# Kernel optimization log

Measured on AMD Instinct MI355X. Metric: run time of the kernel, lower is better.

The kernel has to match this reference:

```python
import jax, jax.numpy as jnp
import numpy as np

B, S, D, H = 2, 2048, 1024, 16
HD = D // H  # head_size = 64

def setup_inputs() -> dict:
    key = jax.random.key(0)
    ks = jax.random.split(key, 8)
    sc = 0.02
    return {
        "q": jax.random.normal(ks[0], (B, S, D), jnp.float32),
        "k": jax.random.normal(ks[1], (B, S, D), jnp.float32),
        "v": jax.random.normal(ks[2], (B, S, D), jnp.float32),
        "padding_mask": jnp.zeros((B, 1, 1, S), jnp.float32),
        "Wq": jax.random.normal(ks[3], (D, D), jnp.float32) * sc,
        "bq": jnp.zeros((D,), jnp.float32),
        "Wk": jax.random.normal(ks[4], (D, D), jnp.float32) * sc,
        "bk": jnp.zeros((D,), jnp.float32),
        "Wv": jax.random.normal(ks[5], (D, D), jnp.float32) * sc,
        "bv": jnp.zeros((D,), jnp.float32),
        "Wo": jax.random.normal(ks[6], (D, D), jnp.float32) * sc,
        "bo": jnp.zeros((D,), jnp.float32),
    }

def reference(q, k, v, padding_mask, Wq, bq, Wk, bk, Wv, bv, Wo, bo):
    b = q.shape[0]
    qh = (q @ Wq + bq).reshape(b, -1, H, HD)
    kh = (k @ Wk + bk).reshape(b, -1, H, HD)
    vh = (v @ Wv + bv).reshape(b, -1, H, HD)
    # [B, H, Sq, Sk] scores, materialized as in the original
    qk = jnp.einsum('bjhd,bkhd->bhjk', qh, kh) / jnp.sqrt(jnp.float32(HD))
    qk = qk + padding_mask * -1e12
    attn = jax.nn.softmax(qk, axis=-1)
    qkv = jnp.einsum('bhjk,bkhd->bjhd', attn, vh).reshape(b, -1, D)
    return qkv @ Wo + bo
```

## Files before the change

### kernel.cpp

```cpp
#include <hip/hip_runtime.h>
#include <math.h>

typedef __bf16 bf16_t;
typedef __bf16 bf16x8 __attribute__((ext_vector_type(8)));
typedef __bf16 bf16x4v __attribute__((ext_vector_type(4)));
typedef float f32x4 __attribute__((ext_vector_type(4)));
typedef float f32x16 __attribute__((ext_vector_type(16)));

#define LOG2E 1.4426950408889634f
#define MBIAS_C (-1e12f * LOG2E)

#if __has_builtin(__builtin_amdgcn_exp2f)
#define EXP2F(x) __builtin_amdgcn_exp2f(x)
#else
#define EXP2F(x) exp2f(x)
#endif

typedef __attribute__((address_space(1))) const unsigned int g_u32;
typedef __attribute__((address_space(3))) unsigned int l_u32;
__device__ __forceinline__ void load_lds_16B(const void* g, void* l){
  __builtin_amdgcn_global_load_lds((g_u32*)g, (l_u32*)l, 16, 0, 0);
}

__device__ __forceinline__ f32x16 zero16(){
  f32x16 z;
  #pragma unroll
  for (int i = 0; i < 16; i++) z[i] = 0.f;
  return z;
}

typedef union { bf16x4v b4; uint2 u2; } pk8;
typedef union { uint2 h[2]; bf16x8 b8; } pk16;
typedef union { float4 f4[4]; f32x16 v; } cinit_t;

__global__ __launch_bounds__(256) void prep_kernel(const float* __restrict__ q,
                                                   const float* __restrict__ k,
                                                   const float* __restrict__ v,
                                                   const float* __restrict__ Wq,
                                                   const float* __restrict__ Wk,
                                                   const float* __restrict__ Wv,
                                                   const float* __restrict__ Wo,
                                                   bf16_t* __restrict__ qkvin,
                                                   bf16_t* __restrict__ Wcat,
                                                   bf16_t* __restrict__ Wot,
                                                   int cast_blocks){
  __shared__ float T[32][33];
  int id = blockIdx.x, tid = threadIdx.x;
  if (id < cast_blocks){
    int z = id >> 12;
    int i = (id & 4095) * 256 + tid;
    const float* x = (z == 0) ? q : (z == 1) ? k : v;
    float4 f = reinterpret_cast<const float4*>(x)[i];
    bf16x4v w;
    w[0] = (bf16_t)f.x; w[1] = (bf16_t)f.y; w[2] = (bf16_t)f.z; w[3] = (bf16_t)f.w;
    reinterpret_cast<bf16x4v*>(qkvin + (size_t)z * 4194304)[i] = w;
  } else {
    int wid = id - cast_blocks;
    int z = wid >> 10, t = wid & 1023;
    int k0 = (t >> 5) * 32, n0 = (t & 31) * 32;
    int x = tid & 31, y = tid >> 5;
    const float* W = (z == 0) ? Wq : (z == 1) ? Wk : (z == 2) ? Wv : Wo;
    bf16_t* dst = (z < 3) ? (Wcat + (size_t)z * 1024 * 1024) : Wot;
    #pragma unroll
    for (int i = 0; i < 4; i++) T[y + 8*i][x] = W[(size_t)(k0 + y + 8*i) * 1024 + n0 + x];
    __syncthreads();
    #pragma unroll
    for (int i = 0; i < 4; i++) dst[(size_t)(n0 + y + 8*i) * 1024 + k0 + x] = (bf16_t)T[x][y + 8*i];
  }
}

__device__ __forceinline__ void qkv_epilogue(f32x4 (&acc)[4][4], int seg, int n0g, int m0,
                                             int wm, int wn, int l16, int lq,
                                             const float* bias, bf16_t* qp, bf16_t* kp,
                                             bf16_t* Vt){
  if (seg < 2){
    bf16_t* Cp = (seg == 0) ? qp : kp;
    float scale = (seg == 0) ? 0.125f * LOG2E : 1.0f;
    #pragma unroll
    for (int ti = 0; ti < 4; ti++){
      #pragma unroll
      for (int tj = 0; tj < 4; tj++){
        int col = (n0g + wn + tj*16 + l16) & 1023;
        float bvv = bias[col];
        #pragma unroll
        for (int r = 0; r < 4; r++){
          int row = m0 + wm + ti*16 + lq*4 + r;
          Cp[(size_t)row * 1024 + col] = (bf16_t)((acc[ti][tj][r] + bvv) * scale);
        }
      }
    }
  } else {
    int b = m0 >> 11;
    int s0base = (m0 & 2047) + wm;
    #pragma unroll
    for (int ti = 0; ti < 4; ti++){
      #pragma unroll
      for (int tj = 0; tj < 4; tj++){
        int col = (n0g + wn + tj*16 + l16) & 1023;
        float bvv = bias[col];
        int h = col >> 6, d = col & 63;
        int s0 = s0base + ti*16 + lq*4;
        pk8 w;
        #pragma unroll
        for (int r = 0; r < 4; r++) w.b4[r] = (bf16_t)(acc[ti][tj][r] + bvv);
        *reinterpret_cast<uint2*>(&Vt[((size_t)(b*16 + h)*64 + d) * 2048 + s0]) = w.u2;
      }
    }
  }
}

__global__ __launch_bounds__(256) void gemm_qkv_bf(const bf16_t* __restrict__ qkvin,
                                                   const bf16_t* __restrict__ Wcat,
                                                   const float* __restrict__ bq,
                                                   const float* __restrict__ bk,
                                                   const float* __restrict__ bv,
                                                   bf16_t* __restrict__ qp,
                                                   bf16_t* __restrict__ kp,
                                                   bf16_t* __restrict__ Vt){
  const int K = 1024;
  __shared__ __align__(16) bf16_t As[2][128*32];
  __shared__ __align__(16) bf16_t Bs[2][128*32];
  int tid = threadIdx.x, wave = tid >> 6, lane = tid & 63;
  int l16 = lane & 15, lq = lane >> 4;
  int m0  = blockIdx.x * 128;
  int n0g = blockIdx.y * 128;
  int seg = n0g >> 10;
  const bf16_t* A   = qkvin + (size_t)seg * 4194304;
  const float* bias = (seg == 0) ? bq : (seg == 1) ? bk : bv;
  int wm = (wave >> 1) * 64, wn = (wave & 1) * 64;
  int cposR = lq ^ ((l16 >> 2) & 3);
  f32x4 acc[4][4] = {};

  auto stage = [&](int kt, int bsel){
    #pragma unroll
    for (int i = 0; i < 2; i++){
      int u = tid + 256*i;
      int r = u >> 2, cpos = u & 3, cg = cpos ^ ((r >> 2) & 3);
      int ldsoff = (wave*64 + 256*i) * 16;
      load_lds_16B(&A[(size_t)(m0 + r) * K + kt + cg*8], (char*)As[bsel] + ldsoff);
      load_lds_16B(&Wcat[(size_t)(n0g + r) * K + kt + cg*8], (char*)Bs[bsel] + ldsoff);
    }
  };
  auto compute = [&](int cur){
    bf16x8 af[4], bfr[4];
    #pragma unroll
    for (int t = 0; t < 4; t++) af[t]  = *reinterpret_cast<bf16x8*>(&As[cur][(wm + t*16 + l16)*32 + cposR*8]);
    #pragma unroll
    for (int t = 0; t < 4; t++) bfr[t] = *reinterpret_cast<bf16x8*>(&Bs[cur][(wn + t*16 + l16)*32 + cposR*8]);
    #pragma unroll
    for (int ti = 0; ti < 4; ti++)
      #pragma unroll
      for (int tj = 0; tj < 4; tj++)
        acc[ti][tj] = __builtin_amdgcn_mfma_f32_16x16x32_bf16(af[ti], bfr[tj], acc[ti][tj], 0, 0, 0);
  };

  stage(0, 0);
  __syncthreads();
  #pragma unroll 1
  for (int it = 0; it < 32; ++it){
    if (it < 31) stage((it + 1) * 32, (it + 1) & 1);
    compute(it & 1);
    __syncthreads();
  }
  qkv_epilogue(acc, seg, n0g, m0, wm, wn, l16, lq, bias, qp, kp, Vt);
}

__global__ __launch_bounds__(256) void gemm_qkv_f32(const float* __restrict__ qi,
                                                    const float* __restrict__ ki,
                                                    const float* __restrict__ vi,
                                                    const bf16_t* __restrict__ Wcat,
                                                    const float* __restrict__ bq,
                                                    const float* __restrict__ bk,
                                                    const float* __restrict__ bv,
                                                    bf16_t* __restrict__ qp,
                                                    bf16_t* __restrict__ kp,
                                                    bf16_t* __restrict__ Vt){
  const int K = 1024;
  __shared__ __align__(16) float  Asf[128*32];
  __shared__ __align__(16) bf16_t Bs[128*32];
  int tid = threadIdx.x, wave = tid >> 6, lane = tid & 63;
  int l16 = lane & 15, lq = lane >> 4;
  int n0g = blockIdx.x * 128;
  int seg = n0g >> 10;
  const float* A    = (seg == 0) ? qi : (seg == 1) ? ki : vi;
  const float* bias = (seg == 0) ? bq : (seg == 1) ? bk : bv;
  int m0 = blockIdx.y * 128;
  int wm = (wave >> 1) * 64, wn = (wave & 1) * 64;
  int cposR = lq ^ ((l16 >> 2) & 3);
  int ca0 = (2*lq)     ^ (l16 & 7);
  int ca1 = (2*lq + 1) ^ (l16 & 7);
  f32x4 acc[4][4] = {};
  for (int kt = 0; kt < K; kt += 32){
    __syncthreads();
    #pragma unroll
    for (int i = 0; i < 4; i++){
      int u = tid + 256*i;
      int r = u >> 3, cpos = u & 7, cg = cpos ^ (r & 7);
      load_lds_16B(&A[(size_t)(m0 + r) * K + kt + cg*4], (char*)Asf + (wave*64 + 256*i)*16);
    }
    #pragma unroll
    for (int i = 0; i < 2; i++){
      int u = tid + 256*i;
      int r = u >> 2, cpos = u & 3, cg = cpos ^ ((r >> 2) & 3);
      load_lds_16B(&Wcat[(size_t)(n0g + r) * K + kt + cg*8], (char*)Bs + (wave*64 + 256*i)*16);
    }
    __syncthreads();
    bf16x8 af[4], bfr[4];
    #pragma unroll
    for (int t = 0; t < 4; t++){
      int row = wm + t*16 + l16;
      f32x4 x0 = *reinterpret_cast<f32x4*>(&Asf[row*32 + ca0*4]);
      f32x4 x1 = *reinterpret_cast<f32x4*>(&Asf[row*32 + ca1*4]);
      bf16x8 a;
      a[0] = (bf16_t)x0[0]; a[1] = (bf16_t)x0[1]; a[2] = (bf16_t)x0[2]; a[3] = (bf16_t)x0[3];
      a[4] = (bf16_t)x1[0]; a[5] = (bf16_t)x1[1]; a[6] = (bf16_t)x1[2]; a[7] = (bf16_t)x1[3];
      af[t] = a;
    }
    #pragma unroll
    for (int t = 0; t < 4; t++) bfr[t] = *reinterpret_cast<bf16x8*>(&Bs[(wn + t*16 + l16)*32 + cposR*8]);
    #pragma unroll
    for (int ti = 0; ti < 4; ti++)
      #pragma unroll
      for (int tj = 0; tj < 4; tj++)
        acc[ti][tj] = __builtin_amdgcn_mfma_f32_16x16x32_bf16(af[ti], bfr[tj], acc[ti][tj], 0, 0, 0);
  }
  qkv_epilogue(acc, seg, n0g, m0, wm, wn, l16, lq, bias, qp, kp, Vt);
}

__global__ __launch_bounds__(256) void gemm_out(const bf16_t* __restrict__ A,
                                                const bf16_t* __restrict__ Bt,
                                                const float* __restrict__ bias,
                                                float* __restrict__ C){
  const int K = 1024, N = 1024;
  __shared__ __align__(16) bf16_t As[2][128*64];
  __shared__ __align__(16) bf16_t Bs[2][64*64];
  int tid = threadIdx.x, wave = tid >> 6, lane = tid & 63;
  int l16 = lane & 15, lq = lane >> 4;
  int m0 = blockIdx.x * 128, n0 = blockIdx.y * 64;
  int wm = wave * 32;
  f32x4 acc[2][4] = {};

  auto stage = [&](int kt, int bsel){
    #pragma unroll
    for (int i = 0; i < 4; i++){
      int u = tid + 256*i;
      int r = u >> 3, cpos = u & 7, cg = cpos ^ (r & 7);
      load_lds_16B(&A[(size_t)(m0 + r) * K + kt + cg*8], (char*)As[bsel] + (wave*64 + 256*i)*16);
    }
    #pragma unroll
    for (int i = 0; i < 2; i++){
      int u = tid + 256*i;
      int r = u >> 3, cpos = u & 7, cg = cpos ^ (r & 7);
      load_lds_16B(&Bt[(size_t)(n0 + r) * K + kt + cg*8], (char*)Bs[bsel] + (wave*64 + 256*i)*16);
    }
  };
  auto compute = [&](int cur){
    #pragma unroll
    for (int kk = 0; kk < 2; kk++){
      bf16x8 af[2], bfr[4];
      #pragma unroll
      for (int t = 0; t < 2; t++){
        int row = wm + t*16 + l16, cpos = (kk*4 + lq) ^ (l16 & 7);
        af[t] = *reinterpret_cast<bf16x8*>(&As[cur][row*64 + cpos*8]);
      }
      #pragma unroll
      for (int t = 0; t < 4; t++){
        int row = t*16 + l16, cpos = (kk*4 + lq) ^ (l16 & 7);
        bfr[t] = *reinterpret_cast<bf16x8*>(&Bs[cur][row*64 + cpos*8]);
      }
      #pragma unroll
      for (int ti = 0; ti < 2; ti++)
        #pragma unroll
        for (int tj = 0; tj < 4; tj++)
          acc[ti][tj] = __builtin_amdgcn_mfma_f32_16x16x32_bf16(af[ti], bfr[tj], acc[ti][tj], 0, 0, 0);
    }
  };

  stage(0, 0);
  __syncthreads();
  #pragma unroll 1
  for (int it = 0; it < 16; ++it){
    if (it < 15) stage((it + 1) * 64, (it + 1) & 1);
    compute(it & 1);
    __syncthreads();
  }

  #pragma unroll
  for (int ti = 0; ti < 2; ti++){
    #pragma unroll
    for (int tj = 0; tj < 4; tj++){
      int col = n0 + tj*16 + l16;
      float bvv = bias[col];
      #pragma unroll
      for (int r = 0; r < 4; r++){
        int row = m0 + wm + ti*16 + lq*4 + r;
        C[(size_t)row * N + col] = acc[ti][tj][r] + bvv;
      }
    }
  }
}

__global__ __launch_bounds__(512, 4) void attn_kernel(const bf16_t* __restrict__ qp,
                                                      const bf16_t* __restrict__ kp,
                                                      const bf16_t* __restrict__ vt,
                                                      const float* __restrict__ mask,
                                                      bf16_t* __restrict__ ctx){
  const int S = 2048, D = 1024, HD = 64;
  __shared__ __align__(16) char smem[74240];
  float* Lsum  = (float*)(smem + 73728);
  float* Opart = (float*)smem;
  float* Mlw   = (float*)(smem + 65536);
  const float* Ml = Mlw;
  int tid = threadIdx.x, wave = tid >> 6, lane = tid & 63;
  int l32 = lane & 31, H = lane >> 5;
  int qo = wave >> 1, khalf = wave & 1;
  int h = blockIdx.x, b = blockIdx.y, qt = blockIdx.z;
  const bf16_t* Qg = qp + (size_t)b*S*D + h*HD;
  const bf16_t* Kg = kp + (size_t)b*S*D + h*HD;
  const bf16_t* Vg = vt + (size_t)(b*16 + h)*HD*S;
  const float*  Mg = mask + (size_t)b*S;

  auto stage = [&](int kt, int bsel){
    char* Kd = smem + bsel*8192;
    char* Vd = smem + 32768 + bsel*8192;
    int r = tid >> 3, c = tid & 7, cg = c ^ (r & 7);
    int ldsoff = wave * 1024;
    load_lds_16B(&Kg[(size_t)(kt + r) * D + cg*8], Kd + ldsoff);
    load_lds_16B(&Vg[(size_t)r * S + kt + cg*8], Vd + ldsoff);
  };

  int qrow = qt*128 + qo*32 + l32;
  bf16x8 qf[4];
  #pragma unroll
  for (int s = 0; s < 4; s++)
    qf[s] = *reinterpret_cast<const bf16x8*>(&Qg[(size_t)qrow * D + s*16 + 8*H]);

  f32x16 o0 = zero16(), o1 = zero16(), lmm = zero16();
  int krow = khalf*32 + l32;

  pk16 ones;
  ones.h[0].x = 0x3F803F80u; ones.h[0].y = 0x3F803F80u;
  ones.h[1].x = 0x3F803F80u; ones.h[1].y = 0x3F803F80u;

  load_lds_16B(&Mg[(size_t)tid*4], smem + 65536 + wave*1024);
  stage(0, 0);
  stage(64, 1);
  __syncthreads();
  {
    f32x4 mv = *reinterpret_cast<f32x4*>(&Mlw[tid*4]);
    mv *= MBIAS_C;
    *reinterpret_cast<f32x4*>(&Mlw[tid*4]) = mv;
  }
  __syncthreads();

  auto tile_compute = [&](int kt, int cur){
    bf16_t* Ks  = (bf16_t*)(smem + cur*8192);
    bf16_t* Vts = (bf16_t*)(smem + 32768 + cur*8192);
    cinit_t ci;
    #pragma unroll
    for (int g = 0; g < 4; g++)
      ci.f4[g] = *reinterpret_cast<const float4*>(&Ml[kt + khalf*32 + 8*g + 4*H]);
    f32x16 sc;
    __builtin_amdgcn_s_setprio(1);
    #pragma unroll
    for (int s = 0; s < 4; s++){
      int cp = (2*s + H) ^ (l32 & 7);
      bf16x8 kf = *reinterpret_cast<bf16x8*>(&Ks[krow*64 + cp*8]);
      if (s == 0) sc = __builtin_amdgcn_mfma_f32_32x32x16_bf16(kf, qf[0], ci.v, 0, 0, 0);
      else        sc = __builtin_amdgcn_mfma_f32_32x32x16_bf16(kf, qf[s], sc, 0, 0, 0);
    }
    __builtin_amdgcn_s_setprio(0);
    pk8 grp[4];
    #pragma unroll
    for (int g = 0; g < 4; g++){
      float p0 = EXP2F(sc[4*g+0]);
      float p1 = EXP2F(sc[4*g+1]);
      float p2 = EXP2F(sc[4*g+2]);
      float p3 = EXP2F(sc[4*g+3]);
      pk8 w;
      w.b4[0] = (bf16_t)p0; w.b4[1] = (bf16_t)p1; w.b4[2] = (bf16_t)p2; w.b4[3] = (bf16_t)p3;
      grp[g] = w;
    }
    #pragma unroll
    for (int kk = 0; kk < 2; kk++){
      uint2 ga = grp[2*kk].u2;
      uint2 gb = grp[2*kk+1].u2;
      uint2 send = H ? ga : gb;
      uint2 recv;
      recv.x = (unsigned)__shfl_xor((int)send.x, 32);
      recv.y = (unsigned)__shfl_xor((int)send.y, 32);
      pk16 fr;
      fr.h[0] = H ? recv : ga;
      fr.h[1] = H ? gb : recv;
      int cp = (4*khalf + 2*kk + H) ^ (l32 & 7);
      bf16x8 vf0 = *reinterpret_cast<bf16x8*>(&Vts[l32*64 + cp*8]);
      bf16x8 vf1 = *reinterpret_cast<bf16x8*>(&Vts[(32 + l32)*64 + cp*8]);
      __builtin_amdgcn_s_setprio(1);
      o0  = __builtin_amdgcn_mfma_f32_32x32x16_bf16(fr.b8, vf0, o0, 0, 0, 0);
      o1  = __builtin_amdgcn_mfma_f32_32x32x16_bf16(fr.b8, vf1, o1, 0, 0, 0);
      lmm = __builtin_amdgcn_mfma_f32_32x32x16_bf16(fr.b8, ones.b8, lmm, 0, 0, 0);
      __builtin_amdgcn_s_setprio(0);
    }
  };

  #pragma unroll 2
  for (int it = 0; it < 16; ++it){
    int kt = it * 128;
    if (it < 15){
      stage(kt + 128, (2*it + 2) & 3);
      stage(kt + 192, (2*it + 3) & 3);
    }
    tile_compute(kt,      (2*it) & 3);
    tile_compute(kt + 64, (2*it + 1) & 3);
    __syncthreads();
  }

  if (khalf == 1){
    #pragma unroll
    for (int reg = 0; reg < 16; reg++){
      Opart[qo*2048 + reg*64 + lane]        = o0[reg];
      Opart[qo*2048 + 1024 + reg*64 + lane] = o1[reg];
    }
    if (l32 == 0){
      #pragma unroll
      for (int reg = 0; reg < 16; reg++)
        Lsum[qo*32 + (reg & 3) + 8*(reg >> 2) + 4*H] = lmm[reg];
    }
  }
  __syncthreads();
  if (khalf == 0){
    #pragma unroll
    for (int reg = 0; reg < 16; reg++){
      o0[reg] += Opart[qo*2048 + reg*64 + lane];
      o1[reg] += Opart[qo*2048 + 1024 + reg*64 + lane];
    }
    #pragma unroll
    for (int g = 0; g < 4; g++){
      #pragma unroll
      for (int r = 0; r < 4; r++){
        float lf = lmm[4*g + r] + Lsum[qo*32 + 8*g + 4*H + r];
        float inv = 1.f / lf;
        int grow = qt*128 + qo*32 + 8*g + 4*H + r;
        size_t base = (size_t)(b*S + grow) * D + h*HD;
        ctx[base + l32]      = (bf16_t)(o0[4*g + r] * inv);
        ctx[base + 32 + l32] = (bf16_t)(o1[4*g + r] * inv);
      }
    }
  }
}

extern "C" void kernel_launch(void* const* d_in, const int* in_sizes, int n_in,
                              void* d_out, int out_size, void* d_ws, size_t ws_size,
                              hipStream_t stream){
  const float* q    = (const float*)d_in[0];
  const float* k    = (const float*)d_in[1];
  const float* v    = (const float*)d_in[2];
  const float* mask = (const float*)d_in[3];
  const float* Wq   = (const float*)d_in[4];
  const float* bq   = (const float*)d_in[5];
  const float* Wk   = (const float*)d_in[6];
  const float* bk   = (const float*)d_in[7];
  const float* Wv   = (const float*)d_in[8];
  const float* bv   = (const float*)d_in[9];
  const float* Wo   = (const float*)d_in[10];
  const float* bo   = (const float*)d_in[11];

  char* ws = (char*)d_ws;
  bf16_t* qp    = (bf16_t*)(ws);
  bf16_t* kp    = (bf16_t*)(ws + 8388608);
  bf16_t* Vt    = (bf16_t*)(ws + 16777216);
  bf16_t* Wcat  = (bf16_t*)(ws + 25165824);
  bf16_t* Wot   = (bf16_t*)(ws + 31457280);
  bf16_t* ctx   = (bf16_t*)(ws + 41943040);
  bf16_t* qkvin = (bf16_t*)(ws + 33554432);

  if (ws_size >= 58720256){
    prep_kernel<<<dim3(16384), 256, 0, stream>>>(q, k, v, Wq, Wk, Wv, Wo, qkvin, Wcat, Wot, 12288);
    gemm_qkv_bf<<<dim3(32,24), 256, 0, stream>>>(qkvin, Wcat, bq, bk, bv, qp, kp, Vt);
  } else {
    prep_kernel<<<dim3(4096), 256, 0, stream>>>(q, k, v, Wq, Wk, Wv, Wo, qkvin, Wcat, Wot, 0);
    gemm_qkv_f32<<<dim3(24,32), 256, 0, stream>>>(q, k, v, Wcat, bq, bk, bv, qp, kp, Vt);
  }
  attn_kernel<<<dim3(16,2,16), 512, 0, stream>>>(qp, kp, Vt, mask, ctx);
  gemm_out<<<dim3(32,16), 256, 0, stream>>>(ctx, Wot, bo, (float*)d_out);
}
```

Measured before the change: 218.4 us.

## Fuse q/k/v bf16 cast into double-buffered f32-input QKV GEMM

Removes the separate pass that cast q, k, v to bf16 in workspace and always uses the f32-input QKV GEMM, converting to bf16 from LDS. The f32 GEMM gains double-buffered LDS staging with prefetch of the next K tile, and its grid is reordered so M runs along x. This aims to cut the extra global write and read of the cast activations and a kernel launch, at the cost of doubled A-operand traffic and more LDS per block.

Result: slower. 228.1 us (+4.4%).

```diff
diff --git a/kernel.cpp b/kernel.cpp
--- a/kernel.cpp
+++ b/kernel.cpp
@@ -33,40 +33,24 @@
 typedef union { uint2 h[2]; bf16x8 b8; } pk16;
 typedef union { float4 f4[4]; f32x16 v; } cinit_t;
 
-__global__ __launch_bounds__(256) void prep_kernel(const float* __restrict__ q,
-                                                   const float* __restrict__ k,
-                                                   const float* __restrict__ v,
-                                                   const float* __restrict__ Wq,
+__global__ __launch_bounds__(256) void prep_kernel(const float* __restrict__ Wq,
                                                    const float* __restrict__ Wk,
                                                    const float* __restrict__ Wv,
                                                    const float* __restrict__ Wo,
-                                                   bf16_t* __restrict__ qkvin,
                                                    bf16_t* __restrict__ Wcat,
-                                                   bf16_t* __restrict__ Wot,
-                                                   int cast_blocks){
+                                                   bf16_t* __restrict__ Wot){
   __shared__ float T[32][33];
   int id = blockIdx.x, tid = threadIdx.x;
-  if (id < cast_blocks){
-    int z = id >> 12;
-    int i = (id & 4095) * 256 + tid;
-    const float* x = (z == 0) ? q : (z == 1) ? k : v;
-    float4 f = reinterpret_cast<const float4*>(x)[i];
-    bf16x4v w;
-    w[0] = (bf16_t)f.x; w[1] = (bf16_t)f.y; w[2] = (bf16_t)f.z; w[3] = (bf16_t)f.w;
-    reinterpret_cast<bf16x4v*>(qkvin + (size_t)z * 4194304)[i] = w;
-  } else {
-    int wid = id - cast_blocks;
-    int z = wid >> 10, t = wid & 1023;
-    int k0 = (t >> 5) * 32, n0 = (t & 31) * 32;
-    int x = tid & 31, y = tid >> 5;
-    const float* W = (z == 0) ? Wq : (z == 1) ? Wk : (z == 2) ? Wv : Wo;
-    bf16_t* dst = (z < 3) ? (Wcat + (size_t)z * 1024 * 1024) : Wot;
-    #pragma unroll
-    for (int i = 0; i < 4; i++) T[y + 8*i][x] = W[(size_t)(k0 + y + 8*i) * 1024 + n0 + x];
-    __syncthreads();
-    #pragma unroll
-    for (int i = 0; i < 4; i++) dst[(size_t)(n0 + y + 8*i) * 1024 + k0 + x] = (bf16_t)T[x][y + 8*i];
-  }
+  int z = id >> 10, t = id & 1023;
+  int k0 = (t >> 5) * 32, n0 = (t & 31) * 32;
+  int x = tid & 31, y = tid >> 5;
+  const float* W = (z == 0) ? Wq : (z == 1) ? Wk : (z == 2) ? Wv : Wo;
+  bf16_t* dst = (z < 3) ? (Wcat + (size_t)z * 1024 * 1024) : Wot;
+  #pragma unroll
+  for (int i = 0; i < 4; i++) T[y + 8*i][x] = W[(size_t)(k0 + y + 8*i) * 1024 + n0 + x];
+  __syncthreads();
+  #pragma unroll
+  for (int i = 0; i < 4; i++) dst[(size_t)(n0 + y + 8*i) * 1024 + k0 + x] = (bf16_t)T[x][y + 8*i];
 }
 
 __device__ __forceinline__ void qkv_epilogue(f32x4 (&acc)[4][4], int seg, int n0g, int m0,
@@ -107,62 +91,6 @@
       }
     }
   }
-}
-
-__global__ __launch_bounds__(256) void gemm_qkv_bf(const bf16_t* __restrict__ qkvin,
-                                                   const bf16_t* __restrict__ Wcat,
-                                                   const float* __restrict__ bq,
-                                                   const float* __restrict__ bk,
-                                                   const float* __restrict__ bv,
-                                                   bf16_t* __restrict__ qp,
-                                                   bf16_t* __restrict__ kp,
-                                                   bf16_t* __restrict__ Vt){
-  const int K = 1024;
-  __shared__ __align__(16) bf16_t As[2][128*32];
-  __shared__ __align__(16) bf16_t Bs[2][128*32];
-  int tid = threadIdx.x, wave = tid >> 6, lane = tid & 63;
-  int l16 = lane & 15, lq = lane >> 4;
-  int m0  = blockIdx.x * 128;
-  int n0g = blockIdx.y * 128;
-  int seg = n0g >> 10;
-  const bf16_t* A   = qkvin + (size_t)seg * 4194304;
-  const float* bias = (seg == 0) ? bq : (seg == 1) ? bk : bv;
-  int wm = (wave >> 1) * 64, wn = (wave & 1) * 64;
-  int cposR = lq ^ ((l16 >> 2) & 3);
-  f32x4 acc[4][4] = {};
-
-  auto stage = [&](int kt, int bsel){
-    #pragma unroll
-    for (int i = 0; i < 2; i++){
-      int u = tid + 256*i;
-      int r = u >> 2, cpos = u & 3, cg = cpos ^ ((r >> 2) & 3);
-      int ldsoff = (wave*64 + 256*i) * 16;
-      load_lds_16B(&A[(size_t)(m0 + r) * K + kt + cg*8], (char*)As[bsel] + ldsoff);
-      load_lds_16B(&Wcat[(size_t)(n0g + r) * K + kt + cg*8], (char*)Bs[bsel] + ldsoff);
-    }
-  };
-  auto compute = [&](int cur){
-    bf16x8 af[4], bfr[4];
-    #pragma unroll
-    for (int t = 0; t < 4; t++) af[t]  = *reinterpret_cast<bf16x8*>(&As[cur][(wm + t*16 + l16)*32 + cposR*8]);
-    #pragma unroll
-    for (int t = 0; t < 4; t++) bfr[t] = *reinterpret_cast<bf16x8*>(&Bs[cur][(wn + t*16 + l16)*32 + cposR*8]);
-    #pragma unroll
-    for (int ti = 0; ti < 4; ti++)
-      #pragma unroll
-      for (int tj = 0; tj < 4; tj++)
-        acc[ti][tj] = __builtin_amdgcn_mfma_f32_16x16x32_bf16(af[ti], bfr[tj], acc[ti][tj], 0, 0, 0);
-  };
-
-  stage(0, 0);
-  __syncthreads();
-  #pragma unroll 1
-  for (int it = 0; it < 32; ++it){
-    if (it < 31) stage((it + 1) * 32, (it + 1) & 1);
-    compute(it & 1);
-    __syncthreads();
-  }
-  qkv_epilogue(acc, seg, n0g, m0, wm, wn, l16, lq, bias, qp, kp, Vt);
 }
 
 __global__ __launch_bounds__(256) void gemm_qkv_f32(const float* __restrict__ qi,
@@ -176,53 +104,63 @@
                                                     bf16_t* __restrict__ kp,
                                                     bf16_t* __restrict__ Vt){
   const int K = 1024;
-  __shared__ __align__(16) float  Asf[128*32];
-  __shared__ __align__(16) bf16_t Bs[128*32];
+  __shared__ __align__(16) float  Asf[2][128*32];
+  __shared__ __align__(16) bf16_t Bs[2][128*32];
   int tid = threadIdx.x, wave = tid >> 6, lane = tid & 63;
   int l16 = lane & 15, lq = lane >> 4;
-  int n0g = blockIdx.x * 128;
+  int m0  = blockIdx.x * 128;
+  int n0g = blockIdx.y * 128;
   int seg = n0g >> 10;
   const float* A    = (seg == 0) ? qi : (seg == 1) ? ki : vi;
   const float* bias = (seg == 0) ? bq : (seg == 1) ? bk : bv;
-  int m0 = blockIdx.y * 128;
   int wm = (wave >> 1) * 64, wn = (wave & 1) * 64;
   int cposR = lq ^ ((l16 >> 2) & 3);
   int ca0 = (2*lq)     ^ (l16 & 7);
   int ca1 = (2*lq + 1) ^ (l16 & 7);
   f32x4 acc[4][4] = {};
-  for (int kt = 0; kt < K; kt += 32){
-    __syncthreads();
+
+  auto stage = [&](int kt, int bsel){
     #pragma unroll
     for (int i = 0; i < 4; i++){
       int u = tid + 256*i;
       int r = u >> 3, cpos = u & 7, cg = cpos ^ (r & 7);
-      load_lds_16B(&A[(size_t)(m0 + r) * K + kt + cg*4], (char*)Asf + (wave*64 + 256*i)*16);
+      load_lds_16B(&A[(size_t)(m0 + r) * K + kt + cg*4], (char*)Asf[bsel] + (wave*64 + 256*i)*16);
     }
     #pragma unroll
     for (int i = 0; i < 2; i++){
       int u = tid + 256*i;
       int r = u >> 2, cpos = u & 3, cg = cpos ^ ((r >> 2) & 3);
-      load_lds_16B(&Wcat[(size_t)(n0g + r) * K + kt + cg*8], (char*)Bs + (wave*64 + 256*i)*16);
-    }
-    __syncthreads();
+      load_lds_16B(&Wcat[(size_t)(n0g + r) * K + kt + cg*8], (char*)Bs[bsel] + (wave*64 + 256*i)*16);
+    }
+  };
+  auto compute = [&](int cur){
     bf16x8 af[4], bfr[4];
     #pragma unroll
     for (int t = 0; t < 4; t++){
       int row = wm + t*16 + l16;
-      f32x4 x0 = *reinterpret_cast<f32x4*>(&Asf[row*32 + ca0*4]);
-      f32x4 x1 = *reinterpret_cast<f32x4*>(&Asf[row*32 + ca1*4]);
+      f32x4 x0 = *reinterpret_cast<f32x4*>(&Asf[cur][row*32 + ca0*4]);
+      f32x4 x1 = *reinterpret_cast<f32x4*>(&Asf[cur][row*32 + ca1*4]);
       bf16x8 a;
       a[0] = (bf16_t)x0[0]; a[1] = (bf16_t)x0[1]; a[2] = (bf16_t)x0[2]; a[3] = (bf16_t)x0[3];
       a[4] = (bf16_t)x1[0]; a[5] = (bf16_t)x1[1]; a[6] = (bf16_t)x1[2]; a[7] = (bf16_t)x1[3];
       af[t] = a;
     }
     #pragma unroll
-    for (int t = 0; t < 4; t++) bfr[t] = *reinterpret_cast<bf16x8*>(&Bs[(wn + t*16 + l16)*32 + cposR*8]);
+    for (int t = 0; t < 4; t++) bfr[t] = *reinterpret_cast<bf16x8*>(&Bs[cur][(wn + t*16 + l16)*32 + cposR*8]);
     #pragma unroll
     for (int ti = 0; ti < 4; ti++)
       #pragma unroll
       for (int tj = 0; tj < 4; tj++)
         acc[ti][tj] = __builtin_amdgcn_mfma_f32_16x16x32_bf16(af[ti], bfr[tj], acc[ti][tj], 0, 0, 0);
+  };
+
+  stage(0, 0);
+  __syncthreads();
+  #pragma unroll 1
+  for (int it = 0; it < 32; ++it){
+    if (it < 31) stage((it + 1) * 32, (it + 1) & 1);
+    compute(it & 1);
+    __syncthreads();
   }
   qkv_epilogue(acc, seg, n0g, m0, wm, wn, l16, lq, bias, qp, kp, Vt);
 }
@@ -471,16 +409,10 @@
   bf16_t* Vt    = (bf16_t*)(ws + 16777216);
   bf16_t* Wcat  = (bf16_t*)(ws + 25165824);
   bf16_t* Wot   = (bf16_t*)(ws + 31457280);
-  bf16_t* ctx   = (bf16_t*)(ws + 41943040);
-  bf16_t* qkvin = (bf16_t*)(ws + 33554432);
-
-  if (ws_size >= 58720256){
-    prep_kernel<<<dim3(16384), 256, 0, stream>>>(q, k, v, Wq, Wk, Wv, Wo, qkvin, Wcat, Wot, 12288);
-    gemm_qkv_bf<<<dim3(32,24), 256, 0, stream>>>(qkvin, Wcat, bq, bk, bv, qp, kp, Vt);
-  } else {
-    prep_kernel<<<dim3(4096), 256, 0, stream>>>(q, k, v, Wq, Wk, Wv, Wo, qkvin, Wcat, Wot, 0);
-    gemm_qkv_f32<<<dim3(24,32), 256, 0, stream>>>(q, k, v, Wcat, bq, bk, bv, qp, kp, Vt);
-  }
+  bf16_t* ctx   = (bf16_t*)(ws + 33554432);
+
+  prep_kernel<<<dim3(4096), 256, 0, stream>>>(Wq, Wk, Wv, Wo, Wcat, Wot);
+  gemm_qkv_f32<<<dim3(32,24), 256, 0, stream>>>(q, k, v, Wcat, bq, bk, bv, qp, kp, Vt);
   attn_kernel<<<dim3(16,2,16), 512, 0, stream>>>(qp, kp, Vt, mask, ctx);
   gemm_out<<<dim3(32,16), 256, 0, stream>>>(ctx, Wot, bo, (float*)d_out);
 }
```
